# Kernel optimization log

Hardware: AMD Instinct MI355X
Metric: run time of the kernel (lower is better)

Reference implementation:

```python
import jax, jax.numpy as jnp
import numpy as np

K_N = 20          # neighbors (init kwarg k_n)
EPS = 1e-5        # BN / InstanceNorm eps (torch default)


def _conv1x1(x, w, b):
    # x: [B,C,N,K], w: [O,C], b: [O]
    return jnp.einsum('bcnk,oc->bonk', x, w) + b[None, :, None, None]


def _bn(x, g, b):
    # training-mode BatchNorm2d: stats over (B,N,K)
    mean = x.mean(axis=(0, 2, 3), keepdims=True)
    var = x.var(axis=(0, 2, 3), keepdims=True)
    return (x - mean) * jax.lax.rsqrt(var + EPS) * g[None, :, None, None] + b[None, :, None, None]


def _inorm(x):
    # InstanceNorm2d (affine=False): stats over (N,K) per (b,c)
    mean = x.mean(axis=(2, 3), keepdims=True)
    var = x.var(axis=(2, 3), keepdims=True)
    return (x - mean) * jax.lax.rsqrt(var + EPS)


def _knn(x, k):
    # x: [B,C,N] -> idx [B,N,k] of nearest neighbors (excluding self)
    sq = jnp.sum(x * x, axis=1)                                   # [B,N]
    neg_d = 2.0 * jnp.einsum('bcn,bcm->bnm', x, x) - sq[:, :, None] - sq[:, None, :]
    _, idx = jax.lax.top_k(neg_d, k + 1)
    return idx[:, :, 1:]


def _res_block(x, w1, b1, g1, be1, w2, b2, g2, be2):
    # pre=False: residual branch is identity
    out = jax.nn.relu(_bn(_inorm(_conv1x1(x, w1, b1)), g1, be1))
    out = _bn(_inorm(_conv1x1(out, w2, b2)), g2, be2)
    return jax.nn.relu(out + x)


def _forward(data, conv0_w, conv0_b, bn0_g, bn0_b, lin_w, lin_b,
             res_w1, res_b1, res_g1, res_be1, res_w2, res_b2, res_g2, res_be2):
    B, C, N = data.shape
    # graph_feature: degree feature from normalized affinity matrix
    nrm = jnp.linalg.norm(data, axis=1, keepdims=True) + 1e-5
    o = data / nrm
    A = jnp.einsum('bcn,bcm->bnm', o, o)                          # [B,N,N]
    D = (jnp.sum(A, axis=1, keepdims=True) - 1.0) / N             # [B,1,N] (subtract eye diag)
    feat = jnp.concatenate([data, jax.nn.relu(jnp.tanh(D))], axis=1)  # [B,129,N]

    idx = _knn(feat, K_N)                                         # [B,N,k]
    xt = jnp.transpose(feat, (0, 2, 1))                           # [B,N,129]
    gathered = jax.vmap(lambda xb, ib: xb[ib])(xt, idx)           # [B,N,k,129]
    center = xt[:, :, None, :]
    edge = jnp.concatenate([jnp.broadcast_to(center, gathered.shape),
                            center - gathered], axis=3)           # [B,N,k,258]
    edge = jnp.transpose(edge, (0, 3, 1, 2))                      # [B,258,N,k]

    out = jax.nn.relu(_bn(_conv1x1(edge, conv0_w, conv0_b), bn0_g, bn0_b))
    out = jnp.max(out, axis=3, keepdims=True)                     # max_pool2d (1,k) -> [B,128,N,1]
    for i in range(4):
        out = _res_block(out, res_w1[i], res_b1[i], res_g1[i], res_be1[i],
                         res_w2[i], res_b2[i], res_g2[i], res_be2[i])
    logit = _conv1x1(out, lin_w, lin_b)                           # [B,1,N,1]
    return logit.reshape(logit.shape[0], -1)                      # [B,N]


def setup_inputs() -> dict:
    B, C, N = 8, 128, 2048
    key = jax.random.key(0)
    ks = jax.random.split(key, 10)
    s = 0.05
    return {
        'data': jax.random.normal(ks[0], (B, C, N), dtype=jnp.float32),
        'x': jax.random.normal(ks[1], (B, C, N), dtype=jnp.float32),  # unused by module
        'conv0_w': jax.random.normal(ks[2], (128, 258), dtype=jnp.float32) * s,
        'conv0_b': jnp.zeros((128,), dtype=jnp.float32),
        'bn0_g': jnp.ones((128,), dtype=jnp.float32),
        'bn0_b': jnp.zeros((128,), dtype=jnp.float32),
        'lin_w': jax.random.normal(ks[3], (1, 128), dtype=jnp.float32) * s,
        'lin_b': jnp.zeros((1,), dtype=jnp.float32),
        'res_w1': jax.random.normal(ks[4], (4, 128, 128), dtype=jnp.float32) * s,
        'res_b1': jnp.zeros((4, 128), dtype=jnp.float32),
        'res_g1': jnp.ones((4, 128), dtype=jnp.float32),
        'res_be1': jnp.zeros((4, 128), dtype=jnp.float32),
        'res_w2': jax.random.normal(ks[5], (4, 128, 128), dtype=jnp.float32) * s,
        'res_b2': jnp.zeros((4, 128), dtype=jnp.float32),
        'res_g2': jnp.ones((4, 128), dtype=jnp.float32),
        'res_be2': jnp.zeros((4, 128), dtype=jnp.float32),
    }


def reference(data, x, conv0_w, conv0_b, bn0_g, bn0_b, lin_w, lin_b,
              res_w1, res_b1, res_g1, res_be1, res_w2, res_b2, res_g2, res_be2):
    # x is accepted but unused, matching the torch module
    return _forward(data, conv0_w, conv0_b, bn0_g, bn0_b, lin_w, lin_b,
                    res_w1, res_b1, res_g1, res_be1, res_w2, res_b2, res_g2, res_be2)
```

## Files before the change

### kernel.cpp

```cpp
#include <hip/hip_runtime.h>
#include <math.h>
#include <float.h>

#define NB 8
#define NC 128
#define NN 2048
#define KNN 20
#define EPSV 1e-5f

#define S_OFF      0
#define BN0S_OFF   1024
#define RESST_OFF  1280
#define ZERO_CNT   17664
#define NRM_OFF    17664
#define SQN_OFF    34048
#define F1_OFF     50432
#define WCAT_OFF   66816
#define WCOL_OFF   99584
#define F128_OFF   99840
#define PQ_OFF     2463232
#define X_OFF      6657536
#define SLOT_SZ    2097152
#define IDX_OFF    12948992
#define G_OFF      13276672
#define XB_OFF     46831104
#define WS_FLOATS  48928256
#define MMN_OFF    (X_OFF + SLOT_SZ)
#define MMX_OFF    (X_OFF + 2 * SLOT_SZ)

__launch_bounds__(256)
__global__ void k1_fused(const float* __restrict__ data, float* __restrict__ ws) {
    int b = blockIdx.y;
    int n0 = blockIdx.x * 64;
    int tid = threadIdx.x;
    __shared__ float tile[128][65];
    __shared__ float red[4][64];
    __shared__ float Linv[64];
    int g = tid >> 6, nn = tid & 63;
    const float* dp = data + (size_t)b * NC * NN + n0 + nn;
    float sq = 0.f;
    for (int c = g; c < 128; c += 4) {
        float v = dp[(size_t)c * NN];
        tile[c][nn] = v;
        sq = fmaf(v, v, sq);
    }
    red[g][nn] = sq;
    __syncthreads();
    if (tid < 64) {
        float s = red[0][tid] + red[1][tid] + red[2][tid] + red[3][tid];
        ws[NRM_OFF + b * NN + n0 + tid] = s;
        Linv[tid] = 1.f / (sqrtf(s) + 1e-5f);
    }
    __syncthreads();
    if (tid < 128) {
        float s = 0.f;
#pragma unroll 8
        for (int j = 0; j < 64; ++j) s = fmaf(tile[tid][j], Linv[j], s);
        atomicAdd(&ws[S_OFF + b * NC + tid], s);
    }
}

__launch_bounds__(256)
__global__ void k2_feat(const float* __restrict__ data, float* __restrict__ ws) {
    int b = blockIdx.y;
    int n0 = blockIdx.x * 64;
    int tid = threadIdx.x;
    __shared__ float Sb[NC];
    __shared__ float fT[64][129];
    __shared__ float redD[4][64];
    if (tid < NC) Sb[tid] = ws[S_OFF + b * NC + tid];
    __syncthreads();
    int nn = tid & 63, cg = tid >> 6;
    float dotp = 0.f;
    const float* dp = data + (size_t)b * NC * NN + n0 + nn;
    for (int c = cg; c < NC; c += 4) {
        float v = dp[(size_t)c * NN];
        fT[nn][c] = v;
        dotp = fmaf(Sb[c], v, dotp);
    }
    redD[cg][nn] = dotp;
    __syncthreads();
    if (tid < 64) {
        float dt = redD[0][tid] + redD[1][tid] + redD[2][tid] + redD[3][tid];
        float nrmsq = ws[NRM_OFF + b * NN + n0 + tid];
        float nrm = sqrtf(nrmsq) + 1e-5f;
        float D = (dt / nrm - 1.f) * (1.f / (float)NN);
        float f1 = tanhf(D); if (f1 < 0.f) f1 = 0.f;
        ws[F1_OFF + b * NN + n0 + tid] = f1;
        ws[SQN_OFF + b * NN + n0 + tid] = nrmsq + f1 * f1;
    }
    __syncthreads();
    float* out = ws + F128_OFF + (size_t)(b * NN + n0) * 128;
    for (int i = tid; i < 64 * 128; i += 256) out[i] = fT[i >> 7][i & 127];
}

__launch_bounds__(256)
__global__ void k4_wcat(const float* __restrict__ w, float* __restrict__ ws) {
    int i = blockIdx.x * 256 + threadIdx.x;
    if (i < 32768) {
        int o = i >> 7, c = i & 127;
        float v = (o < 128) ? w[o * 258 + c] + w[o * 258 + 129 + c]
                            : w[(o - 128) * 258 + 129 + c];
        ws[WCAT_OFF + i] = v;
    } else if (i < 33024) {
        int o = i - 32768;
        float v = (o < 128) ? w[o * 258 + 128] + w[o * 258 + 257]
                            : w[(o - 128) * 258 + 257];
        ws[WCOL_OFF + o] = v;
    }
}

__launch_bounds__(256)
__global__ void k3_gram(float* __restrict__ ws) {
    __shared__ __align__(16) float As[8][128];
    __shared__ __align__(16) float Bs[8][128];
    int tid = threadIdx.x;
    int b = blockIdx.z;
    int m0 = blockIdx.x * 128, n0 = blockIdx.y * 128;
    const float* F = ws + F128_OFF + (size_t)b * NN * 128;
    float acc[8][8];
#pragma unroll
    for (int i = 0; i < 8; ++i)
#pragma unroll
        for (int j = 0; j < 8; ++j) acc[i][j] = 0.f;
    int rr = tid >> 1, cq = tid & 1;
    int tx = tid & 15, ty = tid >> 4;
    for (int kc = 0; kc < 128; kc += 8) {
        float4 av = *(const float4*)&F[(size_t)(n0 + rr) * 128 + kc + cq * 4];
        float4 bv = *(const float4*)&F[(size_t)(m0 + rr) * 128 + kc + cq * 4];
        __syncthreads();
        As[cq*4+0][rr] = av.x; As[cq*4+1][rr] = av.y; As[cq*4+2][rr] = av.z; As[cq*4+3][rr] = av.w;
        Bs[cq*4+0][rr] = bv.x; Bs[cq*4+1][rr] = bv.y; Bs[cq*4+2][rr] = bv.z; Bs[cq*4+3][rr] = bv.w;
        __syncthreads();
#pragma unroll
        for (int kk = 0; kk < 8; ++kk) {
            float a[8], bb[8];
            *(float4*)&a[0]  = *(const float4*)&As[kk][ty * 8];
            *(float4*)&a[4]  = *(const float4*)&As[kk][ty * 8 + 4];
            *(float4*)&bb[0] = *(const float4*)&Bs[kk][tx * 4];
            *(float4*)&bb[4] = *(const float4*)&Bs[kk][64 + tx * 4];
#pragma unroll
            for (int i = 0; i < 8; ++i)
#pragma unroll
                for (int j = 0; j < 8; ++j) acc[i][j] = fmaf(a[i], bb[j], acc[i][j]);
        }
    }
    float sqv[8], f1m[8];
    const float* F1 = ws + F1_OFF + b * NN;
#pragma unroll
    for (int j = 0; j < 4; ++j) {
        sqv[j]     = ws[SQN_OFF + b * NN + m0 + tx * 4 + j];
        sqv[4 + j] = ws[SQN_OFF + b * NN + m0 + 64 + tx * 4 + j];
        f1m[j]     = F1[m0 + tx * 4 + j];
        f1m[4 + j] = F1[m0 + 64 + tx * 4 + j];
    }
    float* G = ws + G_OFF + (size_t)b * NN * NN;
#pragma unroll
    for (int i = 0; i < 8; ++i) {
        int row = n0 + ty * 8 + i;
        float f1n = F1[row];
        float4 o1, o2;
        o1.x = 2.f*fmaf(f1n, f1m[0], acc[i][0]) - sqv[0];
        o1.y = 2.f*fmaf(f1n, f1m[1], acc[i][1]) - sqv[1];
        o1.z = 2.f*fmaf(f1n, f1m[2], acc[i][2]) - sqv[2];
        o1.w = 2.f*fmaf(f1n, f1m[3], acc[i][3]) - sqv[3];
        o2.x = 2.f*fmaf(f1n, f1m[4], acc[i][4]) - sqv[4];
        o2.y = 2.f*fmaf(f1n, f1m[5], acc[i][5]) - sqv[5];
        o2.z = 2.f*fmaf(f1n, f1m[6], acc[i][6]) - sqv[6];
        o2.w = 2.f*fmaf(f1n, f1m[7], acc[i][7]) - sqv[7];
        *(float4*)&G[(size_t)row * NN + m0 + tx * 4]      = o1;
        *(float4*)&G[(size_t)row * NN + m0 + 64 + tx * 4] = o2;
    }
}

__launch_bounds__(256)
__global__ void ksel(float* __restrict__ ws) {
    int wid = threadIdx.x >> 6, lane = threadIdx.x & 63;
    int r = blockIdx.x * 4 + wid;
    const float* row = ws + G_OFF + (size_t)r * NN;
    float v[32];
#pragma unroll
    for (int i = 0; i < 8; ++i)
        *(float4*)&v[i * 4] = *(const float4*)&row[lane * 32 + i * 4];
    float b1v = -FLT_MAX, b2v = -FLT_MAX;
    int b1i = 0, b2i = 0;
#pragma unroll
    for (int i = 0; i < 32; ++i) {
        float x = v[i];
        if (x > b1v)      { b2v = b1v; b2i = b1i; b1v = x; b1i = i; }
        else if (x > b2v) { b2v = x; b2i = i; }
    }
    unsigned int mask = 0u;
    bool has2 = true;
    int* out = (int*)(ws + IDX_OFF) + (size_t)r * KNN;
    for (int k = 0; k < 21; ++k) {
        float M = b1v;
#pragma unroll
        for (int off = 1; off < 64; off <<= 1) M = fmaxf(M, __shfl_xor(M, off));
        unsigned long long tied = __ballot(b1v == M);
        int mm;
        if (__popcll(tied) > 1) {
            int cand = (b1v == M) ? ((lane << 5) | b1i) : 0x7FFFFFFF;
#pragma unroll
            for (int off = 1; off < 64; off <<= 1) {
                int oc = __shfl_xor(cand, off);
                cand = oc < cand ? oc : cand;
            }
            mm = cand;
        } else {
            int l = __ffsll(tied) - 1;
            mm = (l << 5) | __shfl(b1i, l);
        }
        if (k > 0 && lane == 0) out[k - 1] = mm;
        if (lane == (mm >> 5)) {
            mask |= 1u << b1i;
            if (has2) { b1v = b2v; b1i = b2i; has2 = false; }
            else {
                b1v = -FLT_MAX; b2v = -FLT_MAX; b1i = 0; b2i = 0;
#pragma unroll
                for (int i = 0; i < 32; ++i) {
                    float x = (mask & (1u << i)) ? -FLT_MAX : v[i];
                    if (x > b1v)      { b2v = b1v; b2i = b1i; b1v = x; b1i = i; }
                    else if (x > b2v) { b2v = x; b2i = i; }
                }
                has2 = true;
            }
        }
    }
}

__launch_bounds__(256)
__global__ void k5_pq(float* __restrict__ ws) {
    __shared__ __align__(16) float As[16][64];
    __shared__ __align__(16) float Bs[16][64];
    int tid = threadIdx.x;
    int m0 = blockIdx.x * 64, o0 = blockIdx.y * 64;
    int rr = tid >> 2, cq = tid & 3;
    int tx = tid & 15, ty = tid >> 4;
    float acc[4][4];
#pragma unroll
    for (int i = 0; i < 4; ++i)
#pragma unroll
        for (int j = 0; j < 4; ++j) acc[i][j] = 0.f;
    const float* F  = ws + F128_OFF;
    const float* Wc = ws + WCAT_OFF;
    for (int kc = 0; kc < 128; kc += 16) {
        float4 av = *(const float4*)&F [(size_t)(m0 + rr) * 128 + kc + cq * 4];
        float4 bv = *(const float4*)&Wc[(size_t)(o0 + rr) * 128 + kc + cq * 4];
        __syncthreads();
        As[cq*4+0][rr]=av.x; As[cq*4+1][rr]=av.y; As[cq*4+2][rr]=av.z; As[cq*4+3][rr]=av.w;
        Bs[cq*4+0][rr]=bv.x; Bs[cq*4+1][rr]=bv.y; Bs[cq*4+2][rr]=bv.z; Bs[cq*4+3][rr]=bv.w;
        __syncthreads();
#pragma unroll
        for (int kk = 0; kk < 16; ++kk) {
            float a[4], bb[4];
            *(float4*)&a[0]  = *(const float4*)&As[kk][ty * 4];
            *(float4*)&bb[0] = *(const float4*)&Bs[kk][tx * 4];
#pragma unroll
            for (int i = 0; i < 4; ++i)
#pragma unroll
                for (int j = 0; j < 4; ++j) acc[i][j] = fmaf(a[i], bb[j], acc[i][j]);
        }
    }
    float wc[4], f1v[4];
#pragma unroll
    for (int j = 0; j < 4; ++j) {
        wc[j]  = ws[WCOL_OFF + o0 + tx * 4 + j];
        f1v[j] = ws[F1_OFF + m0 + ty * 4 + j];
    }
#pragma unroll
    for (int i = 0; i < 4; ++i) {
        float4 o;
        o.x = fmaf(f1v[i], wc[0], acc[i][0]);
        o.y = fmaf(f1v[i], wc[1], acc[i][1]);
        o.z = fmaf(f1v[i], wc[2], acc[i][2]);
        o.w = fmaf(f1v[i], wc[3], acc[i][3]);
        *(float4*)&ws[PQ_OFF + (size_t)(m0 + ty * 4 + i) * 256 + o0 + tx * 4] = o;
    }
}

__launch_bounds__(256)
__global__ void k6_bn0stats(float* __restrict__ ws) {
    int tid = threadIdx.x;
    int o = tid & 127, h = tid >> 7;
    int m0 = blockIdx.x * 16;
    const float* PQ = ws + PQ_OFF;
    const int* idx = (const int*)(ws + IDX_OFF);
    float* MMn = ws + MMN_OFF;
    float* MMx = ws + MMX_OFF;
    __shared__ float red[2][128];
    float s = 0.f, q = 0.f;
    for (int p = h; p < 16; p += 2) {
        int m = m0 + p;
        int bb = m >> 11;
        float pv = PQ[(size_t)m * 256 + o];
        const int* ip = idx + (size_t)m * KNN;
        float mn = FLT_MAX, mx = -FLT_MAX;
        for (int k = 0; k < KNN; ++k) {
            int j = ip[k];
            float val = pv - PQ[(size_t)(bb * NN + j) * 256 + 128 + o];
            s += val; q += val * val;
            mn = fminf(mn, val); mx = fmaxf(mx, val);
        }
        MMn[(size_t)m * NC + o] = mn;
        MMx[(size_t)m * NC + o] = mx;
    }
    red[h][o] = s; __syncthreads();
    if (tid < 128) atomicAdd(&ws[BN0S_OFF + tid], red[0][tid] + red[1][tid]);
    __syncthreads();
    red[h][o] = q; __syncthreads();
    if (tid < 128) atomicAdd(&ws[BN0S_OFF + 128 + tid], red[0][tid] + red[1][tid]);
}

__launch_bounds__(256)
__global__ void k8_apply(float* __restrict__ ws, const float* __restrict__ g,
                         const float* __restrict__ be) {
    int e = blockIdx.x * 256 + threadIdx.x;
    int fi = e * 4;
    int o = fi & 127;
    const float cnt = 1.f / (float)(NB * NN * KNN);
    float4 sum4 = *(const float4*)&ws[BN0S_OFF + o];
    float4 ssq4 = *(const float4*)&ws[BN0S_OFF + 128 + o];
    float4 g4   = *(const float4*)&g[o];
    float4 be4  = *(const float4*)&be[o];
    float4 mn = *(const float4*)&ws[MMN_OFF + fi];
    float4 mx = *(const float4*)&ws[MMX_OFF + fi];
    float4 r;
#define BN0_DO(comp) { \
    float m_ = sum4.comp * cnt; \
    float v_ = ssq4.comp * cnt - m_ * m_; if (v_ < 0.f) v_ = 0.f; \
    float sc_ = g4.comp * rsqrtf(v_ + EPSV); \
    float sh_ = be4.comp - m_ * sc_; \
    r.comp = fmaxf(fmaf(sc_ > 0.f ? mx.comp : mn.comp, sc_, sh_), 0.f); }
    BN0_DO(x) BN0_DO(y) BN0_DO(z) BN0_DO(w)
#undef BN0_DO
    *(float4*)&ws[X_OFF + fi] = r;
}

__launch_bounds__(256)
__global__ void k9f_conv(const float* __restrict__ x, const float* __restrict__ w,
                         float* __restrict__ y, float* __restrict__ stats,
                         const float* __restrict__ statsIn,
                         const float* __restrict__ g, const float* __restrict__ be,
                         const float* __restrict__ xin, float* __restrict__ xw) {
    __shared__ __align__(16) float As[16][64];
    __shared__ __align__(16) float Bs[16][64];
    __shared__ float red[16][64];
    __shared__ float vvv[8][128];
    __shared__ float scs[128], shs[128];
    int tid = threadIdx.x;
    int m0 = blockIdx.x * 64, o0 = blockIdx.y * 64;
    int bA = m0 >> 11;
    if (statsIn) {
        for (int e = tid; e < 1024; e += 256) {
            float sum = statsIn[e], ssq = statsIn[1024 + e];
            float m_ = sum * (1.f / (float)NN);
            float v_ = ssq * (1.f / (float)NN) - m_ * m_; if (v_ < 0.f) v_ = 0.f;
            vvv[e >> 7][e & 127] = v_ / (v_ + EPSV);
        }
        __syncthreads();
        if (tid < 128) {
            float a = 0.f;
#pragma unroll
            for (int b2 = 0; b2 < NB; ++b2) a += vvv[b2][tid];
            float rsbn = rsqrtf(a * (1.f / (float)NB) + EPSV);
            float sum = statsIn[bA * 128 + tid], ssq = statsIn[1024 + bA * 128 + tid];
            float m_ = sum * (1.f / (float)NN);
            float v_ = ssq * (1.f / (float)NN) - m_ * m_; if (v_ < 0.f) v_ = 0.f;
            float sc_ = rsqrtf(v_ + EPSV) * rsbn * g[tid];
            scs[tid] = sc_;
            shs[tid] = be[tid] - m_ * sc_;
        }
        __syncthreads();
    }
    int rr = tid >> 2, cq = tid & 3;
    int tx = tid & 15, ty = tid >> 4;
    float acc[4][4];
#pragma unroll
    for (int i = 0; i < 4; ++i)
#pragma unroll
        for (int j = 0; j < 4; ++j) acc[i][j] = 0.f;
    for (int kc = 0; kc < NC; kc += 16) {
        float4 av = *(const float4*)&x[(size_t)(m0 + rr) * NC + kc + cq * 4];
        if (statsIn) {
            int c = kc + cq * 4;
            av.x = fmaf(av.x, scs[c],     shs[c]);
            av.y = fmaf(av.y, scs[c + 1], shs[c + 1]);
            av.z = fmaf(av.z, scs[c + 2], shs[c + 2]);
            av.w = fmaf(av.w, scs[c + 3], shs[c + 3]);
            if (xin) {
                float4 xv = *(const float4*)&xin[(size_t)(m0 + rr) * NC + kc + cq * 4];
                av.x += xv.x; av.y += xv.y; av.z += xv.z; av.w += xv.w;
            }
            av.x = fmaxf(av.x, 0.f); av.y = fmaxf(av.y, 0.f);
            av.z = fmaxf(av.z, 0.f); av.w = fmaxf(av.w, 0.f);
            if (xw && blockIdx.y == 0)
                *(float4*)&xw[(size_t)(m0 + rr) * NC + kc + cq * 4] = av;
        }
        float4 bv = *(const float4*)&w[(size_t)(o0 + rr) * NC + kc + cq * 4];
        __syncthreads();
        As[cq*4+0][rr]=av.x; As[cq*4+1][rr]=av.y; As[cq*4+2][rr]=av.z; As[cq*4+3][rr]=av.w;
        Bs[cq*4+0][rr]=bv.x; Bs[cq*4+1][rr]=bv.y; Bs[cq*4+2][rr]=bv.z; Bs[cq*4+3][rr]=bv.w;
        __syncthreads();
#pragma unroll
        for (int kk = 0; kk < 16; ++kk) {
            float a[4], bb[4];
            *(float4*)&a[0]  = *(const float4*)&As[kk][ty * 4];
            *(float4*)&bb[0] = *(const float4*)&Bs[kk][tx * 4];
#pragma unroll
            for (int i = 0; i < 4; ++i)
#pragma unroll
                for (int j = 0; j < 4; ++j) acc[i][j] = fmaf(a[i], bb[j], acc[i][j]);
        }
    }
#pragma unroll
    for (int i = 0; i < 4; ++i) {
        float4 o;
        o.x = acc[i][0]; o.y = acc[i][1]; o.z = acc[i][2]; o.w = acc[i][3];
        *(float4*)&y[(size_t)(m0 + ty * 4 + i) * NC + o0 + tx * 4] = o;
    }
    float s[4], q[4];
#pragma unroll
    for (int j = 0; j < 4; ++j) {
        s[j] = acc[0][j] + acc[1][j] + acc[2][j] + acc[3][j];
        q[j] = acc[0][j]*acc[0][j] + acc[1][j]*acc[1][j] + acc[2][j]*acc[2][j] + acc[3][j]*acc[3][j];
    }
    *(float4*)&red[ty][tx * 4] = make_float4(s[0], s[1], s[2], s[3]);
    __syncthreads();
    if (tid < 64) {
        float t = 0.f;
#pragma unroll
        for (int g2 = 0; g2 < 16; ++g2) t += red[g2][tid];
        atomicAdd(&stats[bA * NC + o0 + tid], t);
    }
    __syncthreads();
    *(float4*)&red[ty][tx * 4] = make_float4(q[0], q[1], q[2], q[3]);
    __syncthreads();
    if (tid < 64) {
        float t = 0.f;
#pragma unroll
        for (int g2 = 0; g2 < 16; ++g2) t += red[g2][tid];
        atomicAdd(&stats[1024 + bA * NC + o0 + tid], t);
    }
}

__launch_bounds__(256)
__global__ void k12_logit(const float* __restrict__ y2, const float* __restrict__ xin,
                          const float* __restrict__ statsIn,
                          const float* __restrict__ g, const float* __restrict__ be,
                          const float* __restrict__ lw, const float* __restrict__ lb,
                          float* __restrict__ out) {
    __shared__ float wsh[128];
    __shared__ float vvv[8][128];
    __shared__ float scs[128], shs[128];
    int tid = threadIdx.x;
    int b = (blockIdx.x * 256) >> 11;
    if (tid < 128) wsh[tid] = lw[tid];
    for (int e = tid; e < 1024; e += 256) {
        float sum = statsIn[e], ssq = statsIn[1024 + e];
        float m_ = sum * (1.f / (float)NN);
        float v_ = ssq * (1.f / (float)NN) - m_ * m_; if (v_ < 0.f) v_ = 0.f;
        vvv[e >> 7][e & 127] = v_ / (v_ + EPSV);
    }
    __syncthreads();
    if (tid < 128) {
        float a = 0.f;
#pragma unroll
        for (int b2 = 0; b2 < NB; ++b2) a += vvv[b2][tid];
        float rsbn = rsqrtf(a * (1.f / (float)NB) + EPSV);
        float sum = statsIn[b * 128 + tid], ssq = statsIn[1024 + b * 128 + tid];
        float m_ = sum * (1.f / (float)NN);
        float v_ = ssq * (1.f / (float)NN) - m_ * m_; if (v_ < 0.f) v_ = 0.f;
        float sc_ = rsqrtf(v_ + EPSV) * rsbn * g[tid];
        scs[tid] = sc_;
        shs[tid] = be[tid] - m_ * sc_;
    }
    __syncthreads();
    int m = blockIdx.x * 256 + tid;
    const float* yp = y2 + (size_t)m * NC;
    const float* xp = xin + (size_t)m * NC;
    float acc = lb[0];
    for (int c = 0; c < NC; c += 4) {
        float4 yv = *(const float4*)&yp[c];
        float4 xv = *(const float4*)&xp[c];
        float v0 = fmaxf(fmaf(yv.x, scs[c],     shs[c])     + xv.x, 0.f);
        float v1 = fmaxf(fmaf(yv.y, scs[c + 1], shs[c + 1]) + xv.y, 0.f);
        float v2 = fmaxf(fmaf(yv.z, scs[c + 2], shs[c + 2]) + xv.z, 0.f);
        float v3 = fmaxf(fmaf(yv.w, scs[c + 3], shs[c + 3]) + xv.w, 0.f);
        acc += v0 * wsh[c] + v1 * wsh[c + 1] + v2 * wsh[c + 2] + v3 * wsh[c + 3];
    }
    out[m] = acc;
}

extern "C" void kernel_launch(void* const* d_in, const int* in_sizes, int n_in,
                              void* d_out, int out_size, void* d_ws, size_t ws_size,
                              hipStream_t stream) {
    if (ws_size < (size_t)WS_FLOATS * 4) return;
    const float* data    = (const float*)d_in[0];
    const float* conv0_w = (const float*)d_in[2];
    const float* bn0_g   = (const float*)d_in[4];
    const float* bn0_b   = (const float*)d_in[5];
    const float* lin_w   = (const float*)d_in[6];
    const float* lin_b   = (const float*)d_in[7];
    const float* res_w1  = (const float*)d_in[8];
    const float* res_g1  = (const float*)d_in[10];
    const float* res_be1 = (const float*)d_in[11];
    const float* res_w2  = (const float*)d_in[12];
    const float* res_g2  = (const float*)d_in[14];
    const float* res_be2 = (const float*)d_in[15];
    float* ws  = (float*)d_ws;
    float* out = (float*)d_out;

    hipMemsetAsync(d_ws, 0, ZERO_CNT * sizeof(float), stream);
    k1_fused<<<dim3(32, 8), 256, 0, stream>>>(data, ws);
    k2_feat<<<dim3(32, 8), 256, 0, stream>>>(data, ws);
    k4_wcat<<<130, 256, 0, stream>>>(conv0_w, ws);
    k3_gram<<<dim3(16, 16, 8), 256, 0, stream>>>(ws);
    ksel<<<4096, 256, 0, stream>>>(ws);
    k5_pq<<<dim3(256, 4), 256, 0, stream>>>(ws);
    k6_bn0stats<<<1024, 256, 0, stream>>>(ws);
    k8_apply<<<2048, 256, 0, stream>>>(ws, bn0_g, bn0_b);

    float* XA = ws + X_OFF;
    float* Y1 = ws + X_OFF + SLOT_SZ;
    float* Y2 = ws + X_OFF + 2 * SLOT_SZ;
    float* XB = ws + XB_OFF;
    float* ST = ws + RESST_OFF;

    k9f_conv<<<dim3(256, 2), 256, 0, stream>>>(XA, res_w1, Y1, ST,
                                               nullptr, nullptr, nullptr, nullptr, nullptr);
    k9f_conv<<<dim3(256, 2), 256, 0, stream>>>(Y1, res_w2, Y2, ST + 2048,
                                               ST, res_g1, res_be1, nullptr, nullptr);
    float* xcur = XA; float* xnext = XB;
    for (int i = 1; i < 4; ++i) {
        int L = 2 * i, L2 = 2 * i + 1;
        k9f_conv<<<dim3(256, 2), 256, 0, stream>>>(Y2, res_w1 + i * 16384, Y1, ST + L * 2048,
                                                   ST + (L - 1) * 2048,
                                                   res_g2 + (i - 1) * 128, res_be2 + (i - 1) * 128,
                                                   xcur, xnext);
        k9f_conv<<<dim3(256, 2), 256, 0, stream>>>(Y1, res_w2 + i * 16384, Y2, ST + L2 * 2048,
                                                   ST + L * 2048,
                                                   res_g1 + i * 128, res_be1 + i * 128,
                                                   nullptr, nullptr);
        float* t = xcur; xcur = xnext; xnext = t;
    }
    k12_logit<<<64, 256, 0, stream>>>(Y2, xcur, ST + 7 * 2048, res_g2 + 3 * 128, res_be2 + 3 * 128,
                                      lin_w, lin_b, out);
}
```

Before: 407.5 us.

## Exploit Gram matrix symmetry by computing only upper-triangle tiles

The kNN distance kernel now launches 136 tiles per batch, covering only the upper triangle of 128x128 blocks, instead of the full 16x16 grid. Each off-diagonal tile writes both its block and the transposed block, using per-row norms loaded for both sides. This roughly halves the matmul FLOPs in the Gram kernel. The transposed writes are less coalesced (each thread writes 8 floats per column row), and the linear-to-triangle index decode uses a small loop.

Result: faster. 378.7 us (-7.1%).

```diff
diff --git a/kernel.cpp b/kernel.cpp
--- a/kernel.cpp
+++ b/kernel.cpp
@@ -116,7 +116,10 @@
     __shared__ __align__(16) float Bs[8][128];
     int tid = threadIdx.x;
     int b = blockIdx.z;
-    int m0 = blockIdx.x * 128, n0 = blockIdx.y * 128;
+    int t = blockIdx.x, a = 0, rem = 16;
+    while (t >= rem) { t -= rem; ++a; --rem; }
+    int bq = a + t;
+    int n0 = a * 128, m0 = bq * 128;
     const float* F = ws + F128_OFF + (size_t)b * NN * 128;
     float acc[8][8];
 #pragma unroll
@@ -134,31 +137,38 @@
         __syncthreads();
 #pragma unroll
         for (int kk = 0; kk < 8; ++kk) {
-            float a[8], bb[8];
-            *(float4*)&a[0]  = *(const float4*)&As[kk][ty * 8];
-            *(float4*)&a[4]  = *(const float4*)&As[kk][ty * 8 + 4];
+            float aa[8], bb[8];
+            *(float4*)&aa[0] = *(const float4*)&As[kk][ty * 8];
+            *(float4*)&aa[4] = *(const float4*)&As[kk][ty * 8 + 4];
             *(float4*)&bb[0] = *(const float4*)&Bs[kk][tx * 4];
             *(float4*)&bb[4] = *(const float4*)&Bs[kk][64 + tx * 4];
 #pragma unroll
             for (int i = 0; i < 8; ++i)
 #pragma unroll
-                for (int j = 0; j < 8; ++j) acc[i][j] = fmaf(a[i], bb[j], acc[i][j]);
-        }
-    }
-    float sqv[8], f1m[8];
+                for (int j = 0; j < 8; ++j) acc[i][j] = fmaf(aa[i], bb[j], acc[i][j]);
+        }
+    }
     const float* F1 = ws + F1_OFF + b * NN;
+    const float* SQ = ws + SQN_OFF + b * NN;
+    float sqv[8], f1m[8], sqn[8], f1nv[8];
 #pragma unroll
     for (int j = 0; j < 4; ++j) {
-        sqv[j]     = ws[SQN_OFF + b * NN + m0 + tx * 4 + j];
-        sqv[4 + j] = ws[SQN_OFF + b * NN + m0 + 64 + tx * 4 + j];
+        sqv[j]     = SQ[m0 + tx * 4 + j];
+        sqv[4 + j] = SQ[m0 + 64 + tx * 4 + j];
         f1m[j]     = F1[m0 + tx * 4 + j];
         f1m[4 + j] = F1[m0 + 64 + tx * 4 + j];
     }
+#pragma unroll
+    for (int i = 0; i < 8; ++i) {
+        int n = n0 + ty * 8 + i;
+        sqn[i]  = SQ[n];
+        f1nv[i] = F1[n];
+    }
     float* G = ws + G_OFF + (size_t)b * NN * NN;
 #pragma unroll
     for (int i = 0; i < 8; ++i) {
         int row = n0 + ty * 8 + i;
-        float f1n = F1[row];
+        float f1n = f1nv[i];
         float4 o1, o2;
         o1.x = 2.f*fmaf(f1n, f1m[0], acc[i][0]) - sqv[0];
         o1.y = 2.f*fmaf(f1n, f1m[1], acc[i][1]) - sqv[1];
@@ -170,6 +180,25 @@
         o2.w = 2.f*fmaf(f1n, f1m[7], acc[i][7]) - sqv[7];
         *(float4*)&G[(size_t)row * NN + m0 + tx * 4]      = o1;
         *(float4*)&G[(size_t)row * NN + m0 + 64 + tx * 4] = o2;
+    }
+    if (a != bq) {
+#pragma unroll
+        for (int j = 0; j < 8; ++j) {
+            int cl = (j < 4) ? (tx * 4 + j) : (64 + tx * 4 + (j - 4));
+            size_t grow = (size_t)(m0 + cl) * NN + n0 + ty * 8;
+            float f1mj = f1m[j];
+            float4 t0, t1;
+            t0.x = 2.f*fmaf(f1nv[0], f1mj, acc[0][j]) - sqn[0];
+            t0.y = 2.f*fmaf(f1nv[1], f1mj, acc[1][j]) - sqn[1];
+            t0.z = 2.f*fmaf(f1nv[2], f1mj, acc[2][j]) - sqn[2];
+            t0.w = 2.f*fmaf(f1nv[3], f1mj, acc[3][j]) - sqn[3];
+            t1.x = 2.f*fmaf(f1nv[4], f1mj, acc[4][j]) - sqn[4];
+            t1.y = 2.f*fmaf(f1nv[5], f1mj, acc[5][j]) - sqn[5];
+            t1.z = 2.f*fmaf(f1nv[6], f1mj, acc[6][j]) - sqn[6];
+            t1.w = 2.f*fmaf(f1nv[7], f1mj, acc[7][j]) - sqn[7];
+            *(float4*)&G[grow]     = t0;
+            *(float4*)&G[grow + 4] = t1;
+        }
     }
 }
 
@@ -515,7 +544,7 @@
     k1_fused<<<dim3(32, 8), 256, 0, stream>>>(data, ws);
     k2_feat<<<dim3(32, 8), 256, 0, stream>>>(data, ws);
     k4_wcat<<<130, 256, 0, stream>>>(conv0_w, ws);
-    k3_gram<<<dim3(16, 16, 8), 256, 0, stream>>>(ws);
+    k3_gram<<<dim3(136, 1, 8), 256, 0, stream>>>(ws);
     ksel<<<4096, 256, 0, stream>>>(ws);
     k5_pq<<<dim3(256, 4), 256, 0, stream>>>(ws);
     k6_bn0stats<<<1024, 256, 0, stream>>>(ws);
```
